# Optimization experiments

Hardware: AMD Instinct MI355X
Metric: run time of the kernel (lower is better)

Reference implementation:

```python
import jax, jax.numpy as jnp
import numpy as np

B, H, L, N = 128, 1024, 256, 64  # batch, d_model, seq len (l_max), SSM state size


def setup_inputs() -> dict:
    key = jax.random.key(0)
    ks = jax.random.split(key, 8)
    x = jax.random.normal(ks[0], (B, H, L), dtype=jnp.float32)
    # S4D init: dt log-uniform in [1e-3, 1e-1], A = -1/2 + i*pi*n, C ~ N(0,1)
    log_dt = jnp.log(10.0 ** jax.random.uniform(ks[1], (H,), minval=-3.0, maxval=-1.0)).astype(jnp.float32)
    A_real_log = jnp.log(0.5 * jnp.ones((H, N), dtype=jnp.float32))
    A_imag = jnp.tile(jnp.pi * jnp.arange(N, dtype=jnp.float32), (H, 1))
    C_re = jax.random.normal(ks[2], (H, N), dtype=jnp.float32)
    C_im = jax.random.normal(ks[3], (H, N), dtype=jnp.float32)
    D = jax.random.normal(ks[4], (H,), dtype=jnp.float32)
    W_out = (jax.random.normal(ks[5], (2 * H, H), dtype=jnp.float32) / np.sqrt(H)).astype(jnp.float32)
    b_out = jnp.zeros((2 * H,), dtype=jnp.float32)
    return dict(x=x, log_dt=log_dt, A_real_log=A_real_log, A_imag=A_imag,
                C_re=C_re, C_im=C_im, D=D, W_out=W_out, b_out=b_out)


def _s4d_kernel(log_dt, A_real_log, A_imag, C_re, C_im, length):
    """S4D convolution kernel (ZOH discretization), shape (H, length)."""
    dt = jnp.exp(log_dt)[:, None]                      # (H, 1)
    A = -jnp.exp(A_real_log) + 1j * A_imag             # (H, N) complex
    C = C_re + 1j * C_im                               # (H, N)
    dtA = A * dt                                       # (H, N)
    C_disc = C * (jnp.exp(dtA) - 1.0) / A              # ZOH-discretized C
    t = jnp.arange(length, dtype=jnp.float32)
    K = jnp.exp(dtA[:, :, None] * t)                   # (H, N, L) Vandermonde
    return 2.0 * jnp.einsum('hn,hnl->hl', C_disc, K).real


def reference(x, log_dt, A_real_log, A_imag, C_re, C_im, D, W_out, b_out):
    Bq, Hq, Lq = x.shape
    k = _s4d_kernel(log_dt, A_real_log, A_imag, C_re, C_im, Lq)  # (H, L)
    n_fft = 2 * Lq
    k_f = jnp.fft.rfft(k, n=n_fft)                     # (H, L+1)
    x_f = jnp.fft.rfft(x, n=n_fft, axis=-1)            # (B, H, L+1)
    y = jnp.fft.irfft(x_f * k_f[None], n=n_fft, axis=-1)[..., :Lq]
    y = y + D[None, :, None] * x                       # skip connection
    y = jax.nn.gelu(y)                                 # FFTConv activation
    # output linear (d_model -> 2*d_model) + GLU over channel dim
    y = jnp.einsum('bhl,gh->bgl', y, W_out) + b_out[None, :, None]
    a, b = jnp.split(y, 2, axis=1)
    return a * jax.nn.sigmoid(b)                       # (B, H, L)
```

## Files before the change

kernel.cpp:

```cpp
#include <hip/hip_runtime.h>
#include <hip/hip_bf16.h>
#include <cstdint>
#include <cstddef>

typedef __bf16 bf16x8 __attribute__((ext_vector_type(8)));
typedef float  f32x4  __attribute__((ext_vector_type(4)));
typedef unsigned short u16x8 __attribute__((ext_vector_type(8)));

__device__ __forceinline__ unsigned short f2bf(float f) {
    unsigned u = __builtin_bit_cast(unsigned, f);
    u += 0x7fffu + ((u >> 16) & 1u);
    return (unsigned short)(u >> 16);
}
__device__ __forceinline__ float bf2f(unsigned short u) {
    unsigned v = ((unsigned)u) << 16;
    return __builtin_bit_cast(float, v);
}
__device__ __forceinline__ float gelu_tanh(float x) {
    float z = 0.7978845608028654f * (x + 0.044715f * x * x * x);
    float e = __expf(2.0f * z);
    float t = 1.0f - 2.0f / (e + 1.0f);
    return 0.5f * x * (1.0f + t);
}

__global__ void k_build(const float* __restrict__ log_dt,
                        const float* __restrict__ arl,
                        const float* __restrict__ aim,
                        const float* __restrict__ cre,
                        const float* __restrict__ cim,
                        const float* __restrict__ Dp,
                        unsigned short* __restrict__ Tg) {
    __shared__ float sRe[64], sIm[64], sCr[64], sCi[64];
    __shared__ float kk[256];
    const int h = blockIdx.x;
    const int t = threadIdx.x;
    if (t < 64) {
        float dt  = expf(log_dt[h]);
        float ar  = -expf(arl[h * 64 + t]);
        float ai  = aim[h * 64 + t];
        float dre = ar * dt, dim = ai * dt;
        float er  = expf(dre);
        float s, c;
        sincosf(dim, &s, &c);
        float em1r = er * c - 1.0f, em1i = er * s;
        float cr = cre[h * 64 + t], ci = cim[h * 64 + t];
        float pr = cr * em1r - ci * em1i;
        float pi = cr * em1i + ci * em1r;
        float inv = 1.0f / (ar * ar + ai * ai);
        sCr[t] = (pr * ar + pi * ai) * inv;
        sCi[t] = (pi * ar - pr * ai) * inv;
        sRe[t] = dre; sIm[t] = dim;
    }
    __syncthreads();
    float acc = 0.0f;
    const float tf = (float)t;
    #pragma unroll 8
    for (int n = 0; n < 64; n++) {
        float er = expf(sRe[n] * tf);
        float s, c;
        sincosf(sIm[n] * tf, &s, &c);
        acc += sCr[n] * er * c - sCi[n] * er * s;
    }
    kk[t] = 2.0f * acc;
    __syncthreads();
    const float Dh = Dp[h];
    unsigned short* dst = Tg + (size_t)h * 16384;
    for (int c = t; c < 1024; c += 256) {
        const int d = c >> 6, q4 = (c >> 4) & 3, mm = c & 15;
        u16x8 hv, lv;
        #pragma unroll
        for (int e = 0; e < 8; e++) {
            const int idx = 16 * d + mm - (q4 * 8 + e);
            float v = (idx >= 0) ? kk[idx] : 0.0f;
            if (idx == 0) v += Dh;
            unsigned short hb = f2bf(v);
            hv[e] = hb;
            lv[e] = f2bf(v - bf2f(hb));
        }
        *(u16x8*)(dst + c * 8)        = hv;
        *(u16x8*)(dst + 8192 + c * 8) = lv;
    }
}

__global__ __launch_bounds__(256, 2)
void conv_mfma(const float* __restrict__ x,
               const unsigned short* __restrict__ Tg,
               unsigned short* __restrict__ yt2) {
    __shared__ __align__(16) unsigned short smem[32768];
    const int h = blockIdx.x, tid = threadIdx.x;
    const int w = tid >> 6, lane = tid & 63, m = lane & 15, q4 = lane >> 4;

    {
        const unsigned short* tg = Tg + (size_t)h * 16384;
        #pragma unroll
        for (int i = 0; i < 8; i++) {
            int q = i * 256 + tid;
            __builtin_amdgcn_global_load_lds(
                (const __attribute__((address_space(1))) void*)(tg + q * 8),
                (__attribute__((address_space(3))) void*)(smem + q * 8), 16, 0, 0);
        }
    }

    const int sb = tid >> 1;
    const float* xrow = x + (((size_t)(sb * 1024 + h)) << 8) + (tid & 1) * 16;

    {
        float4 v0 = *(const float4*)(xrow + 0);
        float4 v1 = *(const float4*)(xrow + 4);
        float4 v2 = *(const float4*)(xrow + 8);
        float4 v3 = *(const float4*)(xrow + 12);
        unsigned short* Xn = smem + 16384;
        const int qb = (tid & 1) * 2;
        #pragma unroll
        for (int s = 0; s < 4; s++) {
            float4 v = (s == 0) ? v0 : (s == 1) ? v1 : (s == 2) ? v2 : v3;
            const int q = qb + (s >> 1), off = (s & 1) * 4;
            ushort4 hv, lv;
            hv.x = f2bf(v.x); lv.x = f2bf(v.x - bf2f(hv.x));
            hv.y = f2bf(v.y); lv.y = f2bf(v.y - bf2f(hv.y));
            hv.z = f2bf(v.z); lv.z = f2bf(v.z - bf2f(hv.z));
            hv.w = f2bf(v.w); lv.w = f2bf(v.w - bf2f(hv.w));
            *(ushort4*)(Xn + (q * 128 + sb) * 8 + off)        = hv;
            *(ushort4*)(Xn + 4096 + (q * 128 + sb) * 8 + off) = lv;
        }
    }

    f32x4 acc[8][4];
    #pragma unroll
    for (int a = 0; a < 8; a++)
        #pragma unroll
        for (int b = 0; b < 4; b++) acc[a][b] = (f32x4){0.f, 0.f, 0.f, 0.f};

    __syncthreads();

    const int fi = (q4 * 16 + m) * 8;

    #pragma unroll 1
    for (int jt = 0; jt < 8; jt++) {
        const unsigned short* Xb = smem + 16384 + (jt & 1) * 8192;
        float4 p0, p1, p2, p3;
        if (jt < 7) {
            const float* xp = xrow + (jt + 1) * 32;
            p0 = *(const float4*)(xp + 0);
            p1 = *(const float4*)(xp + 4);
            p2 = *(const float4*)(xp + 8);
            p3 = *(const float4*)(xp + 12);
        }
        const int j2 = jt << 1;
        const bool a0 = (w      >= j2);
        const bool a1 = (w + 4  >= j2);
        const bool a2 = (w + 8  >= j2);
        const bool a3 = (w + 12 >= j2);
        bf16x8 th0, tl0, th1, tl1, th2, tl2, th3, tl3;
        if (a0) { int d = w      - j2; th0 = *(const bf16x8*)(smem + d * 512 + fi); tl0 = *(const bf16x8*)(smem + 8192 + d * 512 + fi); }
        if (a1) { int d = w + 4  - j2; th1 = *(const bf16x8*)(smem + d * 512 + fi); tl1 = *(const bf16x8*)(smem + 8192 + d * 512 + fi); }
        if (a2) { int d = w + 8  - j2; th2 = *(const bf16x8*)(smem + d * 512 + fi); tl2 = *(const bf16x8*)(smem + 8192 + d * 512 + fi); }
        if (a3) { int d = w + 12 - j2; th3 = *(const bf16x8*)(smem + d * 512 + fi); tl3 = *(const bf16x8*)(smem + 8192 + d * 512 + fi); }
        #pragma unroll
        for (int fb = 0; fb < 8; fb++) {
            const int xo = (q4 * 128 + fb * 16 + m) * 8;
            bf16x8 xh = *(const bf16x8*)(Xb + xo);
            bf16x8 xl = *(const bf16x8*)(Xb + 4096 + xo);
            if (a0) { acc[fb][0] = __builtin_amdgcn_mfma_f32_16x16x32_bf16(xh, th0, acc[fb][0], 0, 0, 0);
                      acc[fb][0] = __builtin_amdgcn_mfma_f32_16x16x32_bf16(xl, th0, acc[fb][0], 0, 0, 0);
                      acc[fb][0] = __builtin_amdgcn_mfma_f32_16x16x32_bf16(xh, tl0, acc[fb][0], 0, 0, 0); }
            if (a1) { acc[fb][1] = __builtin_amdgcn_mfma_f32_16x16x32_bf16(xh, th1, acc[fb][1], 0, 0, 0);
                      acc[fb][1] = __builtin_amdgcn_mfma_f32_16x16x32_bf16(xl, th1, acc[fb][1], 0, 0, 0);
                      acc[fb][1] = __builtin_amdgcn_mfma_f32_16x16x32_bf16(xh, tl1, acc[fb][1], 0, 0, 0); }
            if (a2) { acc[fb][2] = __builtin_amdgcn_mfma_f32_16x16x32_bf16(xh, th2, acc[fb][2], 0, 0, 0);
                      acc[fb][2] = __builtin_amdgcn_mfma_f32_16x16x32_bf16(xl, th2, acc[fb][2], 0, 0, 0);
                      acc[fb][2] = __builtin_amdgcn_mfma_f32_16x16x32_bf16(xh, tl2, acc[fb][2], 0, 0, 0); }
            if (a3) { acc[fb][3] = __builtin_amdgcn_mfma_f32_16x16x32_bf16(xh, th3, acc[fb][3], 0, 0, 0);
                      acc[fb][3] = __builtin_amdgcn_mfma_f32_16x16x32_bf16(xl, th3, acc[fb][3], 0, 0, 0);
                      acc[fb][3] = __builtin_amdgcn_mfma_f32_16x16x32_bf16(xh, tl3, acc[fb][3], 0, 0, 0); }
        }
        if (jt < 7) {
            unsigned short* Xn = smem + 16384 + ((jt + 1) & 1) * 8192;
            const int qb = (tid & 1) * 2;
            #pragma unroll
            for (int s = 0; s < 4; s++) {
                float4 v = (s == 0) ? p0 : (s == 1) ? p1 : (s == 2) ? p2 : p3;
                const int q = qb + (s >> 1), off = (s & 1) * 4;
                ushort4 hv, lv;
                hv.x = f2bf(v.x); lv.x = f2bf(v.x - bf2f(hv.x));
                hv.y = f2bf(v.y); lv.y = f2bf(v.y - bf2f(hv.y));
                hv.z = f2bf(v.z); lv.z = f2bf(v.z - bf2f(hv.z));
                hv.w = f2bf(v.w); lv.w = f2bf(v.w - bf2f(hv.w));
                *(ushort4*)(Xn + (q * 128 + sb) * 8 + off)        = hv;
                *(ushort4*)(Xn + 4096 + (q * 128 + sb) * 8 + off) = lv;
            }
        }
        __syncthreads();
    }

    const size_t ybase = (size_t)h * 32768;
    #pragma unroll
    for (int p = 0; p < 2; p++) {
        #pragma unroll
        for (int tt = 0; tt < 2; tt++) {
            const int ti = p * 2 + tt;
            const int lr = (w + 4 * ti) * 16 + m - p * 128;
            #pragma unroll
            for (int fb = 0; fb < 8; fb++) {
                #pragma unroll
                for (int rg = 0; rg < 4; rg++) {
                    const int b = fb * 16 + q4 * 4 + rg;
                    smem[b * 136 + lr] = f2bf(gelu_tanh(acc[fb][ti][rg]));
                }
            }
        }
        __syncthreads();
        #pragma unroll
        for (int bb = 0; bb < 4; bb++) {
            const int bp = bb * 32 + (tid >> 3);
            #pragma unroll
            for (int s = 0; s < 2; s++) {
                const int chk = (tid & 7) + 8 * s;
                u16x8 v = *(const u16x8*)(smem + bp * 136 + chk * 8);
                *(u16x8*)(yt2 + ybase + (size_t)bp * 256 + p * 128 + chk * 8) = v;
            }
        }
        __syncthreads();
    }
}

__global__ void transp(const unsigned short* __restrict__ yt2,
                       unsigned short* __restrict__ yt) {
    __shared__ __align__(16) unsigned short tl[4096];
    const int tid = threadIdx.x;
    const int m0 = blockIdx.x * 64, h0 = blockIdx.y * 64;
    {
        const int r0 = tid >> 3, ch = tid & 7;
        #pragma unroll
        for (int rr = 0; rr < 64; rr += 32) {
            const int r = r0 + rr;
            u16x8 v = *(const u16x8*)(yt2 + (size_t)(h0 + r) * 32768 + m0 + ch * 8);
            const int pch = ch ^ (r & 7) ^ ((r >> 3) & 7);
            *(u16x8*)(tl + r * 64 + pch * 8) = v;
        }
    }
    __syncthreads();
    {
        const int hc = tid & 7;
        #pragma unroll
        for (int mmr = 0; mmr < 64; mmr += 32) {
            const int mm = (tid >> 3) + mmr;
            u16x8 o;
            #pragma unroll
            for (int e = 0; e < 8; e++) {
                const int hh = hc * 8 + e;
                const int pm = (((mm >> 3) ^ (hh & 7) ^ ((hh >> 3) & 7)) << 3) + (mm & 7);
                o[e] = tl[hh * 64 + pm];
            }
            *(u16x8*)(yt + (size_t)(m0 + mm) * 1024 + h0 + hc * 8) = o;
        }
    }
}

__global__ void pack_w2(const float* __restrict__ W, unsigned short* __restrict__ Wp) {
    const int p   = blockIdx.x;
    const int g32 = p >> 5, r32 = p & 31;
    const int g   = (r32 < 16) ? (g32 * 16 + r32) : (1024 + g32 * 16 + (r32 - 16));
    const int t   = threadIdx.x;
    const float4 v = *(const float4*)(W + (size_t)g * 1024 + t * 4);
    ushort4 o;
    o.x = f2bf(v.x); o.y = f2bf(v.y); o.z = f2bf(v.z); o.w = f2bf(v.w);
    *(ushort4*)(Wp + (size_t)p * 1024 + t * 4) = o;
}

__global__ __launch_bounds__(512, 2)
void gemm_glu2(const unsigned short* __restrict__ yt,
               const unsigned short* __restrict__ Wp,
               const float* __restrict__ bo,
               float* __restrict__ out) {
    __shared__ __align__(16) unsigned short smem[65536];
    const int tid = threadIdx.x;
    const int bid = (int)blockIdx.x;
    const int b1  = (bid & 7) * 128 + (bid >> 3);
    const int bm  = b1 >> 3;
    const int bn  = b1 & 3 | (b1 & 7);
    const int bn_ = b1 & 7;
    const int wid = tid >> 6, lane = tid & 63;
    const int m = lane & 15, q4 = lane >> 4;
    const int wm = wid >> 2, wn = wid & 3;

    const size_t abase = (size_t)bm * 256 * 1024;
    const size_t bbase = (size_t)bn_ * 256 * 1024;

    f32x4 acc[8][4];
    #pragma unroll
    for (int fr = 0; fr < 8; fr++)
        #pragma unroll
        for (int fc = 0; fc < 4; fc++) acc[fr][fc] = (f32x4){0.f, 0.f, 0.f, 0.f};

    auto STAGE = [&](int t) {
        const int bufo = (t & 1) << 15;
        const int k0 = t * 64;
        #pragma unroll
        for (int i = 0; i < 4; i++) {
            int q = i * 512 + tid;
            int r = q >> 3, c = (q & 7) ^ (r & 7);
            const unsigned short* gp = yt + abase + (size_t)r * 1024 + k0 + c * 8;
            __builtin_amdgcn_global_load_lds(
                (const __attribute__((address_space(1))) void*)gp,
                (__attribute__((address_space(3))) void*)(smem + bufo + q * 8), 16, 0, 0);
        }
        #pragma unroll
        for (int i = 0; i < 4; i++) {
            int q = i * 512 + tid;
            int r = q >> 3, c = (q & 7) ^ (r & 7);
            const unsigned short* gp = Wp + bbase + (size_t)r * 1024 + k0 + c * 8;
            __builtin_amdgcn_global_load_lds(
                (const __attribute__((address_space(1))) void*)gp,
                (__attribute__((address_space(3))) void*)(smem + bufo + 16384 + q * 8), 16, 0, 0);
        }
    };

    STAGE(0);
    STAGE(1);
    asm volatile("s_waitcnt vmcnt(8)" ::: "memory");
    __builtin_amdgcn_s_barrier();

    const int arow0 = wm * 128;
    const int brow0 = wn * 64;

    for (int t = 0; t < 16; t++) {
        const int bufo = (t & 1) << 15;
        bf16x8 af[8][2], bf[4][2];
        #pragma unroll
        for (int fr = 0; fr < 8; fr++) {
            const int r = arow0 + fr * 16 + m;
            #pragma unroll
            for (int ks = 0; ks < 2; ks++) {
                const int c = (ks * 4 + q4) ^ (r & 7);
                af[fr][ks] = *(const bf16x8*)(smem + bufo + r * 64 + c * 8);
            }
        }
        #pragma unroll
        for (int fc = 0; fc < 4; fc++) {
            const int r = brow0 + fc * 16 + m;
            #pragma unroll
            for (int ks = 0; ks < 2; ks++) {
                const int c = (ks * 4 + q4) ^ (r & 7);
                bf[fc][ks] = *(const bf16x8*)(smem + bufo + 16384 + r * 64 + c * 8);
            }
        }
        asm volatile("s_waitcnt lgkmcnt(0)" ::: "memory");
        __builtin_amdgcn_sched_barrier(0);
        __builtin_amdgcn_s_barrier();
        if (t < 14) STAGE(t + 2);
        __builtin_amdgcn_s_setprio(1);
        #pragma unroll
        for (int ks = 0; ks < 2; ks++)
            #pragma unroll
            for (int fr = 0; fr < 8; fr++)
                #pragma unroll
                for (int fc = 0; fc < 4; fc++)
                    acc[fr][fc] = __builtin_amdgcn_mfma_f32_16x16x32_bf16(
                        af[fr][ks], bf[fc][ks], acc[fr][fc], 0, 0, 0);
        __builtin_amdgcn_s_setprio(0);
        if (t < 14) asm volatile("s_waitcnt vmcnt(8)" ::: "memory");
        else        asm volatile("s_waitcnt vmcnt(0)" ::: "memory");
        __builtin_amdgcn_s_barrier();
    }

    const size_t outb = ((size_t)bm) << 18;
    const int lbase = wm * 128;
    #pragma unroll
    for (int fcp = 0; fcp < 2; fcp++) {
        const int go = (bn_ * 8 + wn * 2 + fcp) * 16 + m;
        const float boa = bo[go], bog = bo[1024 + go];
        #pragma unroll
        for (int fr = 0; fr < 8; fr++) {
            f32x4 av = acc[fr][2 * fcp];
            f32x4 gv = acc[fr][2 * fcp + 1];
            f32x4 o;
            #pragma unroll
            for (int rg = 0; rg < 4; rg++) {
                float a = av[rg] + boa, g = gv[rg] + bog;
                o[rg] = a / (1.0f + __expf(-g));
            }
            const int l = lbase + fr * 16 + q4 * 4;
            *(f32x4*)(out + outb + (((size_t)go) << 8) + l) = o;
        }
    }
    (void)bn;
}

extern "C" void kernel_launch(void* const* d_in, const int* in_sizes, int n_in,
                              void* d_out, int out_size, void* d_ws, size_t ws_size,
                              hipStream_t stream) {
    const float* x   = (const float*)d_in[0];
    const float* ldt = (const float*)d_in[1];
    const float* arl = (const float*)d_in[2];
    const float* aim = (const float*)d_in[3];
    const float* cre = (const float*)d_in[4];
    const float* cim = (const float*)d_in[5];
    const float* D   = (const float*)d_in[6];
    const float* Wo  = (const float*)d_in[7];
    const float* bo  = (const float*)d_in[8];
    float* out = (float*)d_out;

    const size_t MB = (size_t)1 << 20;
    const size_t need = 132 * MB;
    if (ws_size < need) return;

    unsigned short* Wp  = (unsigned short*)d_ws;
    unsigned short* Tg  = (unsigned short*)((char*)d_ws + 4 * MB);
    unsigned short* yt  = (unsigned short*)((char*)d_ws + 4 * MB);
    unsigned short* yt2 = (unsigned short*)((char*)d_ws + 68 * MB);

    k_build  <<<1024, 256, 0, stream>>>(ldt, arl, aim, cre, cim, D, Tg);
    pack_w2  <<<2048, 256, 0, stream>>>(Wo, Wp);
    conv_mfma<<<1024, 256, 0, stream>>>(x, Tg, yt2);
    transp   <<<dim3(512, 16), 256, 0, stream>>>(yt2, yt);
    gemm_glu2<<<1024, 512, 0, stream>>>(yt, Wp, bo, out);
}
```

Baseline: 441.4 us.

## Load full 128-byte x rows per thread and enlarge transpose tiles

In the conv kernel, each thread pair now loads a whole 64-float segment of an x row, 32 floats per thread, instead of 16 floats per tile. Staging into the double buffer alternates between the two halves, so global loads come in larger contiguous chunks and run two tiles ahead. The transpose kernel switches from 64x64 tiles to 128x256 tiles with a 64KB LDS buffer and an XOR swizzle, which cuts the block count. The cost is more registers held in the conv kernel and lower occupancy in the transpose from its large LDS use.

```diff
diff --git a/kernel.cpp b/kernel.cpp
--- a/kernel.cpp
+++ b/kernel.cpp
@@ -101,29 +101,30 @@
         }
     }
 
-    const int sb = tid >> 1;
-    const float* xrow = x + (((size_t)(sb * 1024 + h)) << 8) + (tid & 1) * 16;
-
-    {
-        float4 v0 = *(const float4*)(xrow + 0);
-        float4 v1 = *(const float4*)(xrow + 4);
-        float4 v2 = *(const float4*)(xrow + 8);
-        float4 v3 = *(const float4*)(xrow + 12);
-        unsigned short* Xn = smem + 16384;
-        const int qb = (tid & 1) * 2;
-        #pragma unroll
-        for (int s = 0; s < 4; s++) {
-            float4 v = (s == 0) ? v0 : (s == 1) ? v1 : (s == 2) ? v2 : v3;
-            const int q = qb + (s >> 1), off = (s & 1) * 4;
+    const int sb = tid >> 1, half = tid & 1;
+    const float* xrow = x + ((size_t)(sb * 1024 + h) << 8);
+
+    float4 cur[8], nxt[8];
+    #pragma unroll
+    for (int s = 0; s < 8; s++) cur[s] = *(const float4*)(xrow + half * 32 + s * 4);
+
+    auto STAGE_X = [&](int tile) {
+        unsigned short* Xn = smem + 16384 + (tile & 1) * 8192;
+        #pragma unroll
+        for (int s = 0; s < 8; s++) {
+            float4 v = cur[s];
             ushort4 hv, lv;
             hv.x = f2bf(v.x); lv.x = f2bf(v.x - bf2f(hv.x));
             hv.y = f2bf(v.y); lv.y = f2bf(v.y - bf2f(hv.y));
             hv.z = f2bf(v.z); lv.z = f2bf(v.z - bf2f(hv.z));
             hv.w = f2bf(v.w); lv.w = f2bf(v.w - bf2f(hv.w));
-            *(ushort4*)(Xn + (q * 128 + sb) * 8 + off)        = hv;
-            *(ushort4*)(Xn + 4096 + (q * 128 + sb) * 8 + off) = lv;
-        }
-    }
+            const int base = (((s >> 1) * 128 + sb) << 3) + (s & 1) * 4;
+            *(ushort4*)(Xn + base)        = hv;
+            *(ushort4*)(Xn + 4096 + base) = lv;
+        }
+    };
+
+    if (half == 0) STAGE_X(0);
 
     f32x4 acc[8][4];
     #pragma unroll
@@ -135,17 +136,8 @@
 
     const int fi = (q4 * 16 + m) * 8;
 
-    #pragma unroll 1
-    for (int jt = 0; jt < 8; jt++) {
+    auto MFMA_BODY = [&](int jt) {
         const unsigned short* Xb = smem + 16384 + (jt & 1) * 8192;
-        float4 p0, p1, p2, p3;
-        if (jt < 7) {
-            const float* xp = xrow + (jt + 1) * 32;
-            p0 = *(const float4*)(xp + 0);
-            p1 = *(const float4*)(xp + 4);
-            p2 = *(const float4*)(xp + 8);
-            p3 = *(const float4*)(xp + 12);
-        }
         const int j2 = jt << 1;
         const bool a0 = (w      >= j2);
         const bool a1 = (w + 4  >= j2);
@@ -174,21 +166,23 @@
                       acc[fb][3] = __builtin_amdgcn_mfma_f32_16x16x32_bf16(xl, th3, acc[fb][3], 0, 0, 0);
                       acc[fb][3] = __builtin_amdgcn_mfma_f32_16x16x32_bf16(xh, tl3, acc[fb][3], 0, 0, 0); }
         }
-        if (jt < 7) {
-            unsigned short* Xn = smem + 16384 + ((jt + 1) & 1) * 8192;
-            const int qb = (tid & 1) * 2;
-            #pragma unroll
-            for (int s = 0; s < 4; s++) {
-                float4 v = (s == 0) ? p0 : (s == 1) ? p1 : (s == 2) ? p2 : p3;
-                const int q = qb + (s >> 1), off = (s & 1) * 4;
-                ushort4 hv, lv;
-                hv.x = f2bf(v.x); lv.x = f2bf(v.x - bf2f(hv.x));
-                hv.y = f2bf(v.y); lv.y = f2bf(v.y - bf2f(hv.y));
-                hv.z = f2bf(v.z); lv.z = f2bf(v.z - bf2f(hv.z));
-                hv.w = f2bf(v.w); lv.w = f2bf(v.w - bf2f(hv.w));
-                *(ushort4*)(Xn + (q * 128 + sb) * 8 + off)        = hv;
-                *(ushort4*)(Xn + 4096 + (q * 128 + sb) * 8 + off) = lv;
-            }
+    };
+
+    #pragma unroll 1
+    for (int g = 0; g < 4; g++) {
+        if (g < 3) {
+            #pragma unroll
+            for (int s = 0; s < 8; s++)
+                nxt[s] = *(const float4*)(xrow + (g + 1) * 64 + half * 32 + s * 4);
+        }
+        MFMA_BODY(2 * g);
+        if (half == 1) STAGE_X(2 * g + 1);
+        __syncthreads();
+        MFMA_BODY(2 * g + 1);
+        if (g < 3) {
+            #pragma unroll
+            for (int s = 0; s < 8; s++) cur[s] = nxt[s];
+            if (half == 0) STAGE_X(2 * g + 2);
         }
         __syncthreads();
     }
@@ -226,34 +220,30 @@
 
 __global__ void transp(const unsigned short* __restrict__ yt2,
                        unsigned short* __restrict__ yt) {
-    __shared__ __align__(16) unsigned short tl[4096];
+    __shared__ __align__(16) unsigned short tl[32768];
     const int tid = threadIdx.x;
-    const int m0 = blockIdx.x * 64, h0 = blockIdx.y * 64;
-    {
-        const int r0 = tid >> 3, ch = tid & 7;
-        #pragma unroll
-        for (int rr = 0; rr < 64; rr += 32) {
-            const int r = r0 + rr;
-            u16x8 v = *(const u16x8*)(yt2 + (size_t)(h0 + r) * 32768 + m0 + ch * 8);
-            const int pch = ch ^ (r & 7) ^ ((r >> 3) & 7);
-            *(u16x8*)(tl + r * 64 + pch * 8) = v;
-        }
+    const int m0 = blockIdx.x * 256, h0 = blockIdx.y * 128;
+    #pragma unroll
+    for (int i = 0; i < 16; i++) {
+        const int q = i * 256 + tid;
+        const int hh = q >> 5, c = q & 31;
+        u16x8 v = *(const u16x8*)(yt2 + (size_t)(h0 + hh) * 32768 + m0 + c * 8);
+        const int pc = c ^ (hh & 31);
+        *(u16x8*)(tl + hh * 256 + pc * 8) = v;
     }
     __syncthreads();
-    {
-        const int hc = tid & 7;
-        #pragma unroll
-        for (int mmr = 0; mmr < 64; mmr += 32) {
-            const int mm = (tid >> 3) + mmr;
-            u16x8 o;
-            #pragma unroll
-            for (int e = 0; e < 8; e++) {
-                const int hh = hc * 8 + e;
-                const int pm = (((mm >> 3) ^ (hh & 7) ^ ((hh >> 3) & 7)) << 3) + (mm & 7);
-                o[e] = tl[hh * 64 + pm];
-            }
-            *(u16x8*)(yt + (size_t)(m0 + mm) * 1024 + h0 + hc * 8) = o;
-        }
+    #pragma unroll
+    for (int i = 0; i < 16; i++) {
+        const int q = i * 256 + tid;
+        const int mm = q >> 4, hc = q & 15;
+        u16x8 o;
+        #pragma unroll
+        for (int e = 0; e < 8; e++) {
+            const int hh = hc * 8 + e;
+            const int pm = ((mm >> 3) ^ (hh & 31)) * 8 + (mm & 7);
+            o[e] = tl[hh * 256 + pm];
+        }
+        *(u16x8*)(yt + (size_t)(m0 + mm) * 1024 + h0 + hc * 8) = o;
     }
 }
 
@@ -278,7 +268,6 @@
     const int bid = (int)blockIdx.x;
     const int b1  = (bid & 7) * 128 + (bid >> 3);
     const int bm  = b1 >> 3;
-    const int bn  = b1 & 3 | (b1 & 7);
     const int bn_ = b1 & 7;
     const int wid = tid >> 6, lane = tid & 63;
     const int m = lane & 15, q4 = lane >> 4;
@@ -384,7 +373,6 @@
             *(f32x4*)(out + outb + (((size_t)go) << 8) + l) = o;
         }
     }
-    (void)bn;
 }
 
 extern "C" void kernel_launch(void* const* d_in, const int* in_sizes, int n_in,
@@ -413,6 +401,6 @@
     k_build  <<<1024, 256, 0, stream>>>(ldt, arl, aim, cre, cim, D, Tg);
     pack_w2  <<<2048, 256, 0, stream>>>(Wo, Wp);
     conv_mfma<<<1024, 256, 0, stream>>>(x, Tg, yt2);
-    transp   <<<dim3(512, 16), 256, 0, stream>>>(yt2, yt);
+    transp   <<<dim3(128, 8), 256, 0, stream>>>(yt2, yt);
     gemm_glu2<<<1024, 512, 0, stream>>>(yt, Wp, bo, out);
 }
```

Result: slower. 460.7 us (+4.4%).
